# Optimization experiments

Measured on AMD Instinct MI355X. Metric: run time of the kernel, lower is better.

## Reference

```python
import jax, jax.numpy as jnp
import numpy as np

STRIDE = 1
PAD = 3  # kernel_size // 2


def _dwconv(x, w, stride, pad):
    # x: [N,C,H,W], w: [C,1,k,k], depthwise (feature_group_count = C)
    C = x.shape[1]
    return jax.lax.conv_general_dilated(
        x, w,
        window_strides=(stride, stride),
        padding=[(pad, pad), (pad, pad)],
        dimension_numbers=("NCHW", "OIHW", "NCHW"),
        feature_group_count=C,
    )


def setup_inputs() -> dict:
    key = jax.random.key(0)
    k1, k2 = jax.random.split(key)
    x = jax.random.normal(k1, (16, 384, 64, 64), dtype=jnp.float32)
    # kaiming_normal_(mode='fan_out', nonlinearity='relu'): std = sqrt(2 / fan_out)
    k_sz = 7
    fan_out = 1 * k_sz * k_sz  # out_channels_per_group * k * k for grouped conv
    std = np.sqrt(2.0 / fan_out).astype(np.float32)
    weight = jax.random.normal(k2, (384, 1, k_sz, k_sz), dtype=jnp.float32) * std
    return {"x": x, "weight": weight}


def reference(x, weight):
    # (conv(x,w0)+conv(x,w90)+conv(x,w180)+conv(x,w270))/4 == conv(x, mean of rotated kernels)
    # (convolution is linear in the kernel; bias=None). Same math, one conv launch.
    w_sym = (weight
             + jnp.rot90(weight, k=1, axes=(2, 3))
             + jnp.rot90(weight, k=2, axes=(2, 3))
             + jnp.rot90(weight, k=3, axes=(2, 3))) * 0.25
    return _dwconv(x, w_sym, STRIDE, PAD)
```

## Files before the change

kernel.cpp:

```cpp
#include <hip/hip_runtime.h>
#include <cstddef>


#define BLOCK 256

constexpr int canon_of(int k) {
    const int i = k / 7, j = k % 7;
    const int a = i * 7 + j;
    const int b = j * 7 + (6 - i);
    const int c = (6 - i) * 7 + (6 - j);
    const int d = (6 - j) * 7 + i;
    int m = a;
    if (b < m) m = b;
    if (c < m) m = c;
    if (d < m) m = d;
    return m;
}
struct Tab { int cidx[49]; };
constexpr Tab build_tab() {
    Tab t{};
    int u = 0;
    for (int k = 0; k < 49; ++k)
        if (canon_of(k) == k) { t.cidx[k] = u; ++u; }
    for (int k = 0; k < 49; ++k) t.cidx[k] = t.cidx[canon_of(k)];
    return t;
}
constexpr Tab TAB = build_tab();

__device__ __forceinline__ float dpp_shr1(float v) {
    return __int_as_float(__builtin_amdgcn_update_dpp(
        0, __float_as_int(v), 0x111, 0xF, 0xF, true));
}
__device__ __forceinline__ float dpp_shl1(float v) {
    return __int_as_float(__builtin_amdgcn_update_dpp(
        0, __float_as_int(v), 0x101, 0xF, 0xF, true));
}

__global__ __launch_bounds__(BLOCK) void dwconv7_sym_kernel(
    const float* __restrict__ x, const float* __restrict__ w,
    float* __restrict__ out, int C)
{
    const int tid = threadIdx.x;
    const int p = __builtin_amdgcn_readfirstlane(tid >> 7);
    const int plane = blockIdx.x * 2 + p;
    const int c = plane % C;

    const int idx = tid & 127;
    const int cg = idx & 15;
    const int S  = idx >> 4;
    const int y0 = S << 3;
    const int x0 = cg << 2;
    const float* __restrict__ xp = x + (size_t)plane * 4096 + x0;
    float* __restrict__ ob = out + (size_t)plane * 4096 + y0 * 64 + x0;

    float4 rows[14];
    #pragma unroll
    for (int m = 0; m < 14; ++m) {
        const int row = y0 - 3 + m;
        const int rr = row < 0 ? 0 : (row > 63 ? 63 : row);
        rows[m] = *(const float4*)(xp + rr * 64);
    }

    const float* __restrict__ wc = w + c * 49;
    float wu[13];
    #pragma unroll
    for (int k = 0; k < 49; ++k) {
        if (canon_of(k) == k) {
            const int i = k / 7, j = k % 7;
            wu[TAB.cidx[k]] = 0.25f * (wc[i * 7 + j]
                                     + wc[j * 7 + (6 - i)]
                                     + wc[(6 - i) * 7 + (6 - j)]
                                     + wc[(6 - j) * 7 + i]);
        }
    }

    float acc[8][4];
    #pragma unroll
    for (int t = 0; t < 8; ++t)
        #pragma unroll
        for (int d = 0; d < 4; ++d) acc[t][d] = 0.f;

    #pragma unroll
    for (int m = 0; m < 14; ++m) {
        const int row = y0 - 3 + m;
        float4 b = rows[m];
        if ((unsigned)row >= 64u) {
            b.x = 0.f; b.y = 0.f; b.z = 0.f; b.w = 0.f;
        }
        const float l1 = dpp_shr1(b.y);
        const float l2 = dpp_shr1(b.z);
        const float l3 = dpp_shr1(b.w);
        const float h4 = dpp_shl1(b.x);
        const float h5 = dpp_shl1(b.y);
        const float h6 = dpp_shl1(b.z);
        const float r_[12] = {0.f, l1, l2, l3, b.x, b.y, b.z, b.w,
                              h4, h5, h6, 0.f};
        #pragma unroll
        for (int t = 0; t < 8; ++t) {
            if (t <= m && m <= t + 6) {
                const int i = m - t;
                #pragma unroll
                for (int d = 0; d < 4; ++d)
                    #pragma unroll
                    for (int j = 0; j < 7; ++j)
                        acc[t][d] += r_[d + j + 1] * wu[TAB.cidx[i * 7 + j]];
            }
        }
    }

    #pragma unroll
    for (int t = 0; t < 8; ++t) {
        float4 v;
        v.x = acc[t][0]; v.y = acc[t][1]; v.z = acc[t][2]; v.w = acc[t][3];
        *(float4*)(ob + t * 64) = v;
    }
}

extern "C" void kernel_launch(void* const* d_in, const int* in_sizes, int n_in,
                              void* d_out, int out_size, void* d_ws, size_t ws_size,
                              hipStream_t stream) {
    const float* x = (const float*)d_in[0];
    const float* w = (const float*)d_in[1];
    float* out = (float*)d_out;

    const int planes = in_sizes[0] / 4096;
    const int C = in_sizes[1] / 49;

    dwconv7_sym_kernel<<<dim3(planes / 2), dim3(BLOCK), 0, stream>>>(x, w, out, C);
}
```

Measured before the change: 179.0 us.

## Process four planes per block with double-buffered register prefetch

Each 128-thread block now handles four planes in sequence instead of two planes at once. Two register buffers of input rows and weights alternate, so loads for the next plane are issued while the current plane computes and stores. The aim is to hide global-memory latency within a block. The cost is higher register pressure and a quarter as many blocks, which may lower occupancy.

```diff
diff --git a/kernel.cpp b/kernel.cpp
--- a/kernel.cpp
+++ b/kernel.cpp
@@ -2,7 +2,8 @@
 #include <cstddef>
 
 
-#define BLOCK 256
+#define BLOCK 128
+#define ITER 4
 
 constexpr int canon_of(int k) {
     const int i = k / 7, j = k % 7;
@@ -36,33 +37,18 @@
         0, __float_as_int(v), 0x101, 0xF, 0xF, true));
 }
 
-__global__ __launch_bounds__(BLOCK) void dwconv7_sym_kernel(
-    const float* __restrict__ x, const float* __restrict__ w,
-    float* __restrict__ out, int C)
-{
-    const int tid = threadIdx.x;
-    const int p = __builtin_amdgcn_readfirstlane(tid >> 7);
-    const int plane = blockIdx.x * 2 + p;
-    const int c = plane % C;
-
-    const int idx = tid & 127;
-    const int cg = idx & 15;
-    const int S  = idx >> 4;
-    const int y0 = S << 3;
-    const int x0 = cg << 2;
-    const float* __restrict__ xp = x + (size_t)plane * 4096 + x0;
-    float* __restrict__ ob = out + (size_t)plane * 4096 + y0 * 64 + x0;
-
-    float4 rows[14];
+__device__ __forceinline__ void load_rows(float4 (&r)[14],
+                                          const float* __restrict__ xp, int y0) {
     #pragma unroll
     for (int m = 0; m < 14; ++m) {
         const int row = y0 - 3 + m;
         const int rr = row < 0 ? 0 : (row > 63 ? 63 : row);
-        rows[m] = *(const float4*)(xp + rr * 64);
+        r[m] = *(const float4*)(xp + rr * 64);
     }
+}
 
-    const float* __restrict__ wc = w + c * 49;
-    float wu[13];
+__device__ __forceinline__ void load_wu(float (&wu)[13],
+                                        const float* __restrict__ wc) {
     #pragma unroll
     for (int k = 0; k < 49; ++k) {
         if (canon_of(k) == k) {
@@ -73,7 +59,11 @@
                                      + wc[(6 - j) * 7 + i]);
         }
     }
+}
 
+__device__ __forceinline__ void compute_store(const float4 (&rows)[14],
+                                              const float (&wu)[13],
+                                              float* __restrict__ ob, int y0) {
     float acc[8][4];
     #pragma unroll
     for (int t = 0; t < 8; ++t)
@@ -116,6 +106,40 @@
     }
 }
 
+__global__ __launch_bounds__(BLOCK) void dwconv7_sym_kernel(
+    const float* __restrict__ x, const float* __restrict__ w,
+    float* __restrict__ out, int C)
+{
+    const int tid = threadIdx.x;
+    const int cg = tid & 15;
+    const int S  = tid >> 4;
+    const int y0 = S << 3;
+    const int x0 = cg << 2;
+    const int p0 = blockIdx.x * ITER;
+
+    float4 rA[14], rB[14];
+    float wuA[13], wuB[13];
+
+    load_rows(rA, x + (size_t)(p0 + 0) * 4096 + x0, y0);
+    load_wu(wuA, w + ((p0 + 0) % C) * 49);
+    load_rows(rB, x + (size_t)(p0 + 1) * 4096 + x0, y0);
+    load_wu(wuB, w + ((p0 + 1) % C) * 49);
+
+    #pragma unroll 1
+    for (int it = 0; it < ITER; it += 2) {
+        compute_store(rA, wuA, out + (size_t)(p0 + it) * 4096 + y0 * 64 + x0, y0);
+        if (it + 2 < ITER) {
+            load_rows(rA, x + (size_t)(p0 + it + 2) * 4096 + x0, y0);
+            load_wu(wuA, w + ((p0 + it + 2) % C) * 49);
+        }
+        compute_store(rB, wuB, out + (size_t)(p0 + it + 1) * 4096 + y0 * 64 + x0, y0);
+        if (it + 3 < ITER) {
+            load_rows(rB, x + (size_t)(p0 + it + 3) * 4096 + x0, y0);
+            load_wu(wuB, w + ((p0 + it + 3) % C) * 49);
+        }
+    }
+}
+
 extern "C" void kernel_launch(void* const* d_in, const int* in_sizes, int n_in,
                               void* d_out, int out_size, void* d_ws, size_t ws_size,
                               hipStream_t stream) {
@@ -126,5 +150,5 @@
     const int planes = in_sizes[0] / 4096;
     const int C = in_sizes[1] / 49;
 
-    dwconv7_sym_kernel<<<dim3(planes / 2), dim3(BLOCK), 0, stream>>>(x, w, out, C);
+    dwconv7_sym_kernel<<<dim3(planes / ITER), dim3(BLOCK), 0, stream>>>(x, w, out, C);
 }
```

Result: slower. 188.8 us (+5.5%).
